# Kernel tuning notes

Hardware: AMD Instinct MI355X
Metric: run time of the kernel (lower is better)

The kernel has to match this reference:

```python
import jax, jax.numpy as jnp
import numpy as np

# --- config constants (from init_kwargs) ---
ALPHA = 0.05; SIGMA = 0.2; THETA = 0.3; A = 0.02; B_PAR = 0.1; RHO = 0.5
MULT = 2.0          # config.x_range_final[1]
GAMMA = 0.5         # power-utility exponent: u(x,r)=r*x^g/g, ux=r*x^(g-1)
N_STEPS = 100; T_FINAL = 1.0; DT = T_FINAL / N_STEPS
HID = 64; BATCH = 16384
PEN_SCALE = 100.0; LOWER = 1e-6


def _mlp(W1, b1, W2, b2, W3, b3, s):
    # tiny FeedForwardSubNet: 3 -> HID -> HID -> 1, tanh activations
    h = jnp.tanh(s @ W1 + b1)
    h = jnp.tanh(h @ W2 + b2)
    return h @ W3 + b3


def _penalise(v):
    # penalise_range(v, lower): quadratic hinge below `lower`
    return PEN_SCALE * jnp.square(jnp.maximum(LOWER - v, 0.0))


def setup_inputs() -> dict:
    key = jax.random.key(0)
    ks = jax.random.split(key, 16)
    dw = jax.random.normal(ks[0], (BATCH, 1, N_STEPS), dtype=jnp.float32) * float(np.sqrt(DT))
    X0 = jnp.ones((1,), jnp.float32)
    R0 = jnp.ones((1,), jnp.float32)
    def w(k, shape, fan):
        return jax.random.normal(k, shape, jnp.float32) / np.float32(np.sqrt(fan))
    inp = {"dw": dw, "X0": X0, "R0": R0,
           "pW1": w(ks[1], (3, HID), 3), "pb1": jnp.zeros((HID,), jnp.float32),
           "pW2": w(ks[2], (HID, HID), HID), "pb2": jnp.zeros((HID,), jnp.float32),
           "pW3": w(ks[3], (HID, 1), HID), "pb3": jnp.zeros((1,), jnp.float32),
           "qW1": w(ks[4], (3, HID), 3), "qb1": jnp.zeros((HID,), jnp.float32),
           "qW2": w(ks[5], (HID, HID), HID), "qb2": jnp.zeros((HID,), jnp.float32),
           "qW3": w(ks[6], (HID, 1), HID), "qb3": jnp.zeros((1,), jnp.float32)}
    return inp


def reference(dw, X0, R0, pW1, pb1, pW2, pb2, pW3, pb3, qW1, qb1, qW2, qb2, qW3, qb3):
    Bn = dw.shape[0]
    ones = jnp.ones((Bn, 1), dw.dtype)
    times = jnp.arange(N_STEPS + 1, dtype=dw.dtype) * DT   # [N+1]
    x0 = ones * X0
    R0v = ones * R0
    b_eff = float(np.sign(RHO)) * B_PAR

    # p_0 and dp_0 = d p_0 / d x (per-sample, rowwise independent net)
    def p_of_x(xx):
        st = jnp.concatenate([MULT * times[0] * ones, xx, R0v], 1)
        return _mlp(pW1, pb1, pW2, pb2, pW3, pb3, st)
    p0, p_vjp = jax.vjp(p_of_x, x0)
    (dp0,) = p_vjp(jnp.ones_like(p0))
    pi0 = _mlp(qW1, qb1, qW2, qb2, qW3, qb3,
               jnp.concatenate([MULT * times[0] * ones, x0, R0v], 1))

    dw_t = jnp.transpose(dw, (2, 0, 1))          # [N, B, 1]
    upd = jnp.arange(N_STEPS) < (N_STEPS - 1)    # pi not updated at last step

    def step(carry, inp):
        x, min_x, W, pi = carry
        dwi, t_next, u = inp
        x = x + x * ALPHA * DT + pi * SIGMA * THETA * DT + pi * SIGMA * dwi
        min_x = jnp.minimum(x, min_x)
        W = W + dwi
        Rv = R0v * jnp.exp((A - 0.5 * b_eff ** 2) * t_next + b_eff * W)
        p = p0 * jnp.exp(-(ALPHA + 0.5 * THETA ** 2) * t_next - THETA * W)
        st = jnp.concatenate([MULT * t_next * jnp.ones_like(x), x, Rv], 1)
        pi_new = _mlp(qW1, qb1, qW2, qb2, qW3, qb3, st)
        pi = jnp.where(u, pi_new, pi)
        return (x, min_x, W, pi), (x, Rv, pi, -p)

    (xf, min_x, Wf, pif), (xs, Rs, pis, dMs) = jax.lax.scan(
        step, (x0, x0, jnp.zeros_like(x0), pi0), (dw_t, times[1:], upd))

    # stacked process data, matching tf.concat-over-axis-0 ordering: [(N+1)*B, 1]
    x_all  = jnp.concatenate([x0[None], xs], 0).reshape(-1, 1)
    r_all  = jnp.concatenate([R0v[None], Rs], 0).reshape(-1, 1)
    pi_all = jnp.concatenate([pi0[None], pis], 0).reshape(-1, 1)
    dM_all = jnp.concatenate([(-p0)[None], dMs], 0).reshape(-1, 1)
    dM2_all = jnp.tile(-dp0, (N_STEPS + 1, 1))
    proc = jnp.concatenate([x_all, r_all, pi_all, dM_all, dM2_all], 1)  # [(N+1)*B, 5]

    # losses (non_concave = False branch)
    p_fin = -dMs[-1]
    R_fin = Rs[-1]
    xc = jnp.maximum(xf, LOWER)
    ux = R_fin * xc ** (GAMMA - 1.0)
    u_val = R_fin * xc ** GAMMA / GAMMA
    pen = _penalise(min_x)
    loss_p = jnp.mean(jnp.square(p_fin + ux) + pen)
    loss_pi = loss_p + jnp.mean(-u_val + pen)

    return jnp.concatenate([proc.reshape(-1), jnp.stack([loss_p, loss_pi])])
```

## Files before the change

kernel.cpp:

```cpp
#include <hip/hip_runtime.h>
#include <math.h>

#define NSTEP 100
#define BATCH 16384
#define MB 16
#define NBLK (BATCH/MB)
#define NT 64

#define C_ALPHA 0.05f
#define C_SIGMA 0.2f
#define C_THETA 0.3f
#define C_DT    0.01f
#define C_LOWER 1e-6f
#define C_PEN   100.0f
#define LOG2E   1.4426950408889634f
#define TSCALE  (2.0f * LOG2E)
#define CRT ( 0.015f * C_DT * LOG2E)
#define CRW ( 0.1f * LOG2E)
#define CPT (-0.095f * C_DT * LOG2E)
#define CPW (-0.3f * LOG2E)

typedef __attribute__((ext_vector_type(8))) short bf16x8;
typedef __attribute__((ext_vector_type(4))) float f32x4;

__device__ __forceinline__ float tanh_pre(float zs) {
    float e = __builtin_amdgcn_exp2f(zs);
    return 1.0f - 2.0f * __builtin_amdgcn_rcpf(e + 1.0f);
}
__device__ __forceinline__ unsigned f2bf_u(float f) {
    unsigned u = __float_as_uint(f);
    return (u + 0x7FFFu + ((u >> 16) & 1u)) >> 16;
}

__global__ void init_kernel(const float* X0, const float* R0,
                            const float* pW1, const float* pb1, const float* pW2,
                            const float* pb2, const float* pW3, const float* pb3,
                            const float* qW1, const float* qb1, const float* qW2,
                            const float* qb2, const float* qW3, const float* qb3,
                            float* ws) {
    __shared__ float sw[2][4096];
    int tid = threadIdx.x;
    for (int u = tid; u < 4096; u += 256) { sw[0][u] = pW2[u]; sw[1][u] = qW2[u]; }
    __syncthreads();
    int wv = tid >> 6, j = tid & 63;
    float sx = X0[0], sr = R0[0];
    if (wv == 0) {
        float pre = pW1[64 + j] * sx + pW1[128 + j] * sr + pb1[j];
        float h1 = tanh_pre(TSCALE * pre);
        float d1 = (1.0f - h1 * h1) * pW1[64 + j];
        float pre2 = pb2[j], dpre2 = 0.0f;
        #pragma unroll 8
        for (int i2 = 0; i2 < 64; i2++) {
            float w = sw[0][i2 * 64 + j];
            pre2  += __shfl(h1, i2) * w;
            dpre2 += __shfl(d1, i2) * w;
        }
        float h2 = tanh_pre(TSCALE * pre2);
        float d2 = (1.0f - h2 * h2) * dpre2;
        float c1 = h2 * pW3[j], c2 = d2 * pW3[j];
        for (int o = 32; o >= 1; o >>= 1) {
            c1 += __shfl_down(c1, o); c2 += __shfl_down(c2, o);
        }
        if (j == 0) { ws[0] = c1 + pb3[0]; ws[1] = c2; }
    } else if (wv == 1) {
        float pre = qW1[64 + j] * sx + qW1[128 + j] * sr + qb1[j];
        float h1 = tanh_pre(TSCALE * pre);
        float pre2 = qb2[j];
        #pragma unroll 8
        for (int i2 = 0; i2 < 64; i2++) pre2 += __shfl(h1, i2) * sw[1][i2 * 64 + j];
        float h2 = tanh_pre(TSCALE * pre2);
        float c1 = h2 * qW3[j];
        for (int o = 32; o >= 1; o >>= 1) c1 += __shfl_down(c1, o);
        if (j == 0) { ws[2] = c1 + qb3[0]; ws[3] = 0.0f; ws[4] = 0.0f; ws[5] = 0.0f; }
    }
}

__global__ __launch_bounds__(NT, 1) void step_kernel(
        const float* __restrict__ dw, const float* __restrict__ X0,
        const float* __restrict__ R0,
        const float* __restrict__ qW1, const float* __restrict__ qb1,
        const float* __restrict__ qW2, const float* __restrict__ qb2,
        const float* __restrict__ qW3, const float* __restrict__ qb3,
        float* __restrict__ ws, float* __restrict__ out) {
    __shared__ __align__(16) unsigned short sW2T[64 * 72];
    __shared__ __align__(16) float sdw[MB * NSTEP];
    __shared__ __align__(16) float sPi[MB];

    const int lane = threadIdx.x;
    const int b0 = blockIdx.x * MB;
    const int l15 = lane & 15, quad = lane >> 4;

    {
        const float4* g = (const float4*)(dw + (size_t)b0 * NSTEP);
        float4* s = (float4*)sdw;
        #pragma unroll
        for (int u = lane; u < MB * NSTEP / 4; u += NT) s[u] = g[u];
    }
    #pragma unroll 8
    for (int t = 0; t < 64; t++) {
        float w = qW2[t * 64 + lane];
        sW2T[lane * 72 + t] = (unsigned short)f2bf_u(w * TSCALE);
    }
    bf16x8 Bf[4][2];
    #pragma unroll
    for (int nt = 0; nt < 4; nt++) {
        const unsigned short* r = &sW2T[(nt * 16 + l15) * 72 + quad * 8];
        Bf[nt][0] = *(const bf16x8*)r;
        Bf[nt][1] = *(const bf16x8*)(r + 32);
    }
    float tco[16], w1xs[16], w1rs[16], b1s[16];
    #pragma unroll
    for (int idx = 0; idx < 16; idx++) {
        int k = (idx < 8) ? (quad * 8 + idx) : (32 + quad * 8 + (idx - 8));
        tco[idx]  = qW1[k] * (2.0f * C_DT * TSCALE);
        w1xs[idx] = qW1[64 + k] * TSCALE;
        w1rs[idx] = qW1[128 + k] * TSCALE;
        b1s[idx]  = qb1[k] * TSCALE;
    }
    float b2v[4], w3v[4];
    #pragma unroll
    for (int nt = 0; nt < 4; nt++) {
        b2v[nt] = qb2[nt * 16 + l15] * TSCALE;
        w3v[nt] = qW3[nt * 16 + l15];
    }
    const float b3 = qb3[0];
    const float p0 = ws[0], dp0 = ws[1], pi0 = ws[2];
    const float X0v = X0[0], R0s = R0[0];

    float x = 0.f, Wsum = 0.f, minx = 0.f, R0v = 0.f, pi = 0.f;
    float v1 = 0.f, v2 = 0.f;
    if (lane < MB) {
        x = X0v; R0v = R0s; minx = x; pi = pi0;
        sPi[lane] = pi0;
        size_t base = (size_t)(b0 + lane) * 5;
        out[base] = x; out[base + 1] = R0v; out[base + 2] = pi0;
        out[base + 3] = -p0; out[base + 4] = -dp0;
    }

    #pragma unroll 1
    for (int i = 0; i < NSTEP - 1; i++) {
        float fi = (float)(i + 1);
        float Rcur = 0.f;
        if (lane < MB) {
            pi = sPi[lane];
            float dwv = sdw[lane * NSTEP + i];
            x = x * (1.0f + C_ALPHA * C_DT) + pi * C_SIGMA * (C_THETA * C_DT + dwv);
            minx = fminf(minx, x);
            Wsum += dwv;
            Rcur = R0v * __builtin_amdgcn_exp2f(fmaf(CRW, Wsum, CRT * fi));
            float pm = p0 * __builtin_amdgcn_exp2f(fmaf(CPW, Wsum, CPT * fi));
            size_t base = ((size_t)(i + 1) * BATCH + b0 + lane) * 5;
            out[base] = x; out[base + 1] = Rcur;
            out[base + 3] = -pm; out[base + 4] = -dp0;
        }
        float xb = __shfl(x, l15);
        float rb = __shfl(Rcur, l15);

        union { bf16x8 v; unsigned u[4]; } A0, A1;
        #pragma unroll
        for (int p = 0; p < 8; p++) {
            int i0 = 2 * p, i1 = 2 * p + 1;
            float z0 = fmaf(w1rs[i0], rb, fmaf(w1xs[i0], xb, fmaf(tco[i0], fi, b1s[i0])));
            float z1 = fmaf(w1rs[i1], rb, fmaf(w1xs[i1], xb, fmaf(tco[i1], fi, b1s[i1])));
            unsigned pk = f2bf_u(tanh_pre(z0)) | (f2bf_u(tanh_pre(z1)) << 16);
            if (p < 4) A0.u[p] = pk; else A1.u[p - 4] = pk;
        }
        f32x4 part;
        {
            f32x4 acc0 = {b2v[0], b2v[0], b2v[0], b2v[0]};
            f32x4 acc1 = {b2v[1], b2v[1], b2v[1], b2v[1]};
            f32x4 acc2 = {b2v[2], b2v[2], b2v[2], b2v[2]};
            f32x4 acc3 = {b2v[3], b2v[3], b2v[3], b2v[3]};
            acc0 = __builtin_amdgcn_mfma_f32_16x16x32_bf16(A0.v, Bf[0][0], acc0, 0, 0, 0);
            acc1 = __builtin_amdgcn_mfma_f32_16x16x32_bf16(A0.v, Bf[1][0], acc1, 0, 0, 0);
            acc2 = __builtin_amdgcn_mfma_f32_16x16x32_bf16(A0.v, Bf[2][0], acc2, 0, 0, 0);
            acc3 = __builtin_amdgcn_mfma_f32_16x16x32_bf16(A0.v, Bf[3][0], acc3, 0, 0, 0);
            acc0 = __builtin_amdgcn_mfma_f32_16x16x32_bf16(A1.v, Bf[0][1], acc0, 0, 0, 0);
            acc1 = __builtin_amdgcn_mfma_f32_16x16x32_bf16(A1.v, Bf[1][1], acc1, 0, 0, 0);
            acc2 = __builtin_amdgcn_mfma_f32_16x16x32_bf16(A1.v, Bf[2][1], acc2, 0, 0, 0);
            acc3 = __builtin_amdgcn_mfma_f32_16x16x32_bf16(A1.v, Bf[3][1], acc3, 0, 0, 0);
            #pragma unroll
            for (int r = 0; r < 4; r++) {
                float s = tanh_pre(acc0[r]) * w3v[0];
                s = fmaf(tanh_pre(acc1[r]), w3v[1], s);
                s = fmaf(tanh_pre(acc2[r]), w3v[2], s);
                s = fmaf(tanh_pre(acc3[r]), w3v[3], s);
                part[r] = s;
            }
        }
        #pragma unroll
        for (int o = 1; o < 16; o <<= 1) {
            part[0] += __shfl_xor(part[0], o);
            part[1] += __shfl_xor(part[1], o);
            part[2] += __shfl_xor(part[2], o);
            part[3] += __shfl_xor(part[3], o);
        }
        if (l15 == 0) {
            float q0 = part[0] + b3, q1 = part[1] + b3;
            float q2 = part[2] + b3, q3 = part[3] + b3;
            f32x4 pv = {q0, q1, q2, q3};
            *(f32x4*)&sPi[quad * 4] = pv;
            size_t base = ((size_t)(i + 1) * BATCH + b0 + quad * 4) * 5 + 2;
            out[base] = q0; out[base + 5] = q1; out[base + 10] = q2; out[base + 15] = q3;
        }
    }

    if (lane < MB) {
        pi = sPi[lane];
        float dwv = sdw[lane * NSTEP + (NSTEP - 1)];
        x = x * (1.0f + C_ALPHA * C_DT) + pi * C_SIGMA * (C_THETA * C_DT + dwv);
        minx = fminf(minx, x);
        Wsum += dwv;
        float Rf = R0v * __builtin_amdgcn_exp2f(fmaf(CRW, Wsum, CRT * (float)NSTEP));
        float pf = p0 * __builtin_amdgcn_exp2f(fmaf(CPW, Wsum, CPT * (float)NSTEP));
        size_t base = ((size_t)NSTEP * BATCH + b0 + lane) * 5;
        out[base] = x; out[base + 1] = Rf; out[base + 2] = pi;
        out[base + 3] = -pf; out[base + 4] = -dp0;

        float xc = fmaxf(x, C_LOWER);
        float ux = Rf * rsqrtf(xc);
        float uval = 2.0f * Rf * sqrtf(xc);
        float d = fmaxf(C_LOWER - minx, 0.0f);
        float pen = C_PEN * d * d;
        float t1 = pf + ux;
        v1 = t1 * t1 + pen;
        v2 = -uval + pen;
    }
    #pragma unroll
    for (int o = 8; o >= 1; o >>= 1) {
        v1 += __shfl_down(v1, o);
        v2 += __shfl_down(v2, o);
    }
    if (lane == 0) {
        atomicAdd(&ws[3], v1);
        atomicAdd(&ws[4], v2);
        __threadfence();
        int old = atomicAdd((int*)(ws + 5), 1);
        if (old == NBLK - 1) {
            float lp = atomicAdd(&ws[3], 0.0f) * (1.0f / (float)BATCH);
            float lq = atomicAdd(&ws[4], 0.0f) * (1.0f / (float)BATCH);
            out[(size_t)(NSTEP + 1) * BATCH * 5] = lp;
            out[(size_t)(NSTEP + 1) * BATCH * 5 + 1] = lp + lq;
        }
    }
}

extern "C" void kernel_launch(void* const* d_in, const int* in_sizes, int n_in,
                              void* d_out, int out_size, void* d_ws, size_t ws_size,
                              hipStream_t stream) {
    const float* dw  = (const float*)d_in[0];
    const float* X0  = (const float*)d_in[1];
    const float* R0  = (const float*)d_in[2];
    const float* pW1 = (const float*)d_in[3];
    const float* pb1 = (const float*)d_in[4];
    const float* pW2 = (const float*)d_in[5];
    const float* pb2 = (const float*)d_in[6];
    const float* pW3 = (const float*)d_in[7];
    const float* pb3 = (const float*)d_in[8];
    const float* qW1 = (const float*)d_in[9];
    const float* qb1 = (const float*)d_in[10];
    const float* qW2 = (const float*)d_in[11];
    const float* qb2 = (const float*)d_in[12];
    const float* qW3 = (const float*)d_in[13];
    const float* qb3 = (const float*)d_in[14];
    float* out = (float*)d_out;
    float* ws  = (float*)d_ws;

    init_kernel<<<1, 256, 0, stream>>>(X0, R0, pW1, pb1, pW2, pb2, pW3, pb3,
                                       qW1, qb1, qW2, qb2, qW3, qb3, ws);
    step_kernel<<<NBLK, NT, 0, stream>>>(dw, X0, R0, qW1, qb1, qW2, qb2, qW3, qb3,
                                         ws, out);
}
```

Baseline: 229.0 us.

## Fuse init kernel into step kernel and keep recurrence state replicated across lanes

Drops the separate single-block init kernel: each block now computes p0/dp0 and the initial policy value itself, and the accumulators are zeroed with a memset. The per-step state update runs redundantly in every quad, so the shared-memory round trip for pi is gone. The 16-lane reductions use DPP row operations and the result is redistributed with ds_bpermute instead of shfl_xor chains. dw values are prefetched one step ahead and bf16 packing uses the library intrinsic. In exchange, every block recomputes the small p-net.

Result: faster. 209.6 us (-8.5%).

```diff
diff --git a/kernel.cpp b/kernel.cpp
--- a/kernel.cpp
+++ b/kernel.cpp
@@ -1,4 +1,5 @@
 #include <hip/hip_runtime.h>
+#include <hip/hip_bf16.h>
 #include <math.h>
 
 #define NSTEP 100
@@ -31,60 +32,36 @@
     unsigned u = __float_as_uint(f);
     return (u + 0x7FFFu + ((u >> 16) & 1u)) >> 16;
 }
-
-__global__ void init_kernel(const float* X0, const float* R0,
-                            const float* pW1, const float* pb1, const float* pW2,
-                            const float* pb2, const float* pW3, const float* pb3,
-                            const float* qW1, const float* qb1, const float* qW2,
-                            const float* qb2, const float* qW3, const float* qb3,
-                            float* ws) {
-    __shared__ float sw[2][4096];
-    int tid = threadIdx.x;
-    for (int u = tid; u < 4096; u += 256) { sw[0][u] = pW2[u]; sw[1][u] = qW2[u]; }
-    __syncthreads();
-    int wv = tid >> 6, j = tid & 63;
-    float sx = X0[0], sr = R0[0];
-    if (wv == 0) {
-        float pre = pW1[64 + j] * sx + pW1[128 + j] * sr + pb1[j];
-        float h1 = tanh_pre(TSCALE * pre);
-        float d1 = (1.0f - h1 * h1) * pW1[64 + j];
-        float pre2 = pb2[j], dpre2 = 0.0f;
-        #pragma unroll 8
-        for (int i2 = 0; i2 < 64; i2++) {
-            float w = sw[0][i2 * 64 + j];
-            pre2  += __shfl(h1, i2) * w;
-            dpre2 += __shfl(d1, i2) * w;
-        }
-        float h2 = tanh_pre(TSCALE * pre2);
-        float d2 = (1.0f - h2 * h2) * dpre2;
-        float c1 = h2 * pW3[j], c2 = d2 * pW3[j];
-        for (int o = 32; o >= 1; o >>= 1) {
-            c1 += __shfl_down(c1, o); c2 += __shfl_down(c2, o);
-        }
-        if (j == 0) { ws[0] = c1 + pb3[0]; ws[1] = c2; }
-    } else if (wv == 1) {
-        float pre = qW1[64 + j] * sx + qW1[128 + j] * sr + qb1[j];
-        float h1 = tanh_pre(TSCALE * pre);
-        float pre2 = qb2[j];
-        #pragma unroll 8
-        for (int i2 = 0; i2 < 64; i2++) pre2 += __shfl(h1, i2) * sw[1][i2 * 64 + j];
-        float h2 = tanh_pre(TSCALE * pre2);
-        float c1 = h2 * qW3[j];
-        for (int o = 32; o >= 1; o >>= 1) c1 += __shfl_down(c1, o);
-        if (j == 0) { ws[2] = c1 + qb3[0]; ws[3] = 0.0f; ws[4] = 0.0f; ws[5] = 0.0f; }
-    }
-}
-
-__global__ __launch_bounds__(NT, 1) void step_kernel(
+__device__ __forceinline__ unsigned pack_bf16(float a, float b) {
+    union { __hip_bfloat162 h; unsigned u; } cv;
+    cv.h = __float22bfloat162_rn(make_float2(a, b));
+    return cv.u;
+}
+__device__ __forceinline__ float dpp_row_sum16(float v) {
+    int t;
+    t = __builtin_amdgcn_update_dpp(0, __float_as_int(v), 0x128, 0xF, 0xF, true);
+    v += __int_as_float(t);
+    t = __builtin_amdgcn_update_dpp(0, __float_as_int(v), 0x124, 0xF, 0xF, true);
+    v += __int_as_float(t);
+    t = __builtin_amdgcn_update_dpp(0, __float_as_int(v), 0x122, 0xF, 0xF, true);
+    v += __int_as_float(t);
+    t = __builtin_amdgcn_update_dpp(0, __float_as_int(v), 0x121, 0xF, 0xF, true);
+    v += __int_as_float(t);
+    return v;
+}
+
+__global__ __launch_bounds__(NT, 1) void fused_kernel(
         const float* __restrict__ dw, const float* __restrict__ X0,
         const float* __restrict__ R0,
+        const float* __restrict__ pW1, const float* __restrict__ pb1,
+        const float* __restrict__ pW2, const float* __restrict__ pb2,
+        const float* __restrict__ pW3, const float* __restrict__ pb3,
         const float* __restrict__ qW1, const float* __restrict__ qb1,
         const float* __restrict__ qW2, const float* __restrict__ qb2,
         const float* __restrict__ qW3, const float* __restrict__ qb3,
         float* __restrict__ ws, float* __restrict__ out) {
     __shared__ __align__(16) unsigned short sW2T[64 * 72];
     __shared__ __align__(16) float sdw[MB * NSTEP];
-    __shared__ __align__(16) float sPi[MB];
 
     const int lane = threadIdx.x;
     const int b0 = blockIdx.x * MB;
@@ -97,10 +74,10 @@
         for (int u = lane; u < MB * NSTEP / 4; u += NT) s[u] = g[u];
     }
     #pragma unroll 8
-    for (int t = 0; t < 64; t++) {
-        float w = qW2[t * 64 + lane];
-        sW2T[lane * 72 + t] = (unsigned short)f2bf_u(w * TSCALE);
-    }
+    for (int t = 0; t < 64; t++)
+        sW2T[lane * 72 + t] = (unsigned short)f2bf_u(qW2[t * 64 + lane] * TSCALE);
+    __syncthreads();
+
     bf16x8 Bf[4][2];
     #pragma unroll
     for (int nt = 0; nt < 4; nt++) {
@@ -124,123 +101,136 @@
         w3v[nt] = qW3[nt * 16 + l15];
     }
     const float b3 = qb3[0];
-    const float p0 = ws[0], dp0 = ws[1], pi0 = ws[2];
     const float X0v = X0[0], R0s = R0[0];
-
-    float x = 0.f, Wsum = 0.f, minx = 0.f, R0v = 0.f, pi = 0.f;
-    float v1 = 0.f, v2 = 0.f;
-    if (lane < MB) {
-        x = X0v; R0v = R0s; minx = x; pi = pi0;
-        sPi[lane] = pi0;
-        size_t base = (size_t)(b0 + lane) * 5;
-        out[base] = x; out[base + 1] = R0v; out[base + 2] = pi0;
+    const int bperm_idx = (((l15 >> 2) * 16) + (l15 & 3)) * 4;
+
+    float p0, dp0;
+    {
+        float pre = fmaf(pW1[64 + lane], X0v, fmaf(pW1[128 + lane], R0s, pb1[lane]));
+        float h1 = tanh_pre(TSCALE * pre);
+        float d1 = (1.0f - h1 * h1) * pW1[64 + lane];
+        float a0 = pb2[lane], a1 = 0.f, a2 = 0.f, a3 = 0.f;
+        float e0 = 0.f, e1 = 0.f, e2 = 0.f, e3 = 0.f;
+        for (int i2 = 0; i2 < 64; i2 += 4) {
+            float w0 = pW2[(i2 + 0) * 64 + lane];
+            float w1 = pW2[(i2 + 1) * 64 + lane];
+            float w2 = pW2[(i2 + 2) * 64 + lane];
+            float w3 = pW2[(i2 + 3) * 64 + lane];
+            a0 = fmaf(__shfl(h1, i2 + 0), w0, a0); e0 = fmaf(__shfl(d1, i2 + 0), w0, e0);
+            a1 = fmaf(__shfl(h1, i2 + 1), w1, a1); e1 = fmaf(__shfl(d1, i2 + 1), w1, e1);
+            a2 = fmaf(__shfl(h1, i2 + 2), w2, a2); e2 = fmaf(__shfl(d1, i2 + 2), w2, e2);
+            a3 = fmaf(__shfl(h1, i2 + 3), w3, a3); e3 = fmaf(__shfl(d1, i2 + 3), w3, e3);
+        }
+        float pre2 = (a0 + a1) + (a2 + a3);
+        float dpre2 = (e0 + e1) + (e2 + e3);
+        float h2 = tanh_pre(TSCALE * pre2);
+        float d2 = (1.0f - h2 * h2) * dpre2;
+        float c1 = h2 * pW3[lane], c2 = d2 * pW3[lane];
+        #pragma unroll
+        for (int o = 1; o < 64; o <<= 1) {
+            c1 += __shfl_xor(c1, o);
+            c2 += __shfl_xor(c2, o);
+        }
+        p0 = c1 + pb3[0]; dp0 = c2;
+    }
+
+    auto qnet = [&](float fi, float xv, float rv) -> float {
+        union { bf16x8 v; unsigned u[4]; } A0, A1;
+        #pragma unroll
+        for (int p = 0; p < 8; p++) {
+            const int i0 = 2 * p, i1 = 2 * p + 1;
+            float z0 = fmaf(w1rs[i0], rv, fmaf(w1xs[i0], xv, fmaf(tco[i0], fi, b1s[i0])));
+            float z1 = fmaf(w1rs[i1], rv, fmaf(w1xs[i1], xv, fmaf(tco[i1], fi, b1s[i1])));
+            unsigned pk = pack_bf16(tanh_pre(z0), tanh_pre(z1));
+            if (p < 4) A0.u[p] = pk; else A1.u[p - 4] = pk;
+        }
+        f32x4 acc0 = {b2v[0], b2v[0], b2v[0], b2v[0]};
+        f32x4 acc1 = {b2v[1], b2v[1], b2v[1], b2v[1]};
+        f32x4 acc2 = {b2v[2], b2v[2], b2v[2], b2v[2]};
+        f32x4 acc3 = {b2v[3], b2v[3], b2v[3], b2v[3]};
+        acc0 = __builtin_amdgcn_mfma_f32_16x16x32_bf16(A0.v, Bf[0][0], acc0, 0, 0, 0);
+        acc1 = __builtin_amdgcn_mfma_f32_16x16x32_bf16(A0.v, Bf[1][0], acc1, 0, 0, 0);
+        acc2 = __builtin_amdgcn_mfma_f32_16x16x32_bf16(A0.v, Bf[2][0], acc2, 0, 0, 0);
+        acc3 = __builtin_amdgcn_mfma_f32_16x16x32_bf16(A0.v, Bf[3][0], acc3, 0, 0, 0);
+        acc0 = __builtin_amdgcn_mfma_f32_16x16x32_bf16(A1.v, Bf[0][1], acc0, 0, 0, 0);
+        acc1 = __builtin_amdgcn_mfma_f32_16x16x32_bf16(A1.v, Bf[1][1], acc1, 0, 0, 0);
+        acc2 = __builtin_amdgcn_mfma_f32_16x16x32_bf16(A1.v, Bf[2][1], acc2, 0, 0, 0);
+        acc3 = __builtin_amdgcn_mfma_f32_16x16x32_bf16(A1.v, Bf[3][1], acc3, 0, 0, 0);
+        f32x4 part;
+        #pragma unroll
+        for (int r = 0; r < 4; r++) {
+            float sA = fmaf(tanh_pre(acc1[r]), w3v[1], tanh_pre(acc0[r]) * w3v[0]);
+            float sB = fmaf(tanh_pre(acc3[r]), w3v[3], tanh_pre(acc2[r]) * w3v[2]);
+            part[r] = dpp_row_sum16(sA + sB);
+        }
+        float sLo = (lane & 1) ? part[1] : part[0];
+        float sHi = (lane & 1) ? part[3] : part[2];
+        float sel = (lane & 2) ? sHi : sLo;
+        int g = __builtin_amdgcn_ds_bpermute(bperm_idx, __float_as_int(sel));
+        return __int_as_float(g) + b3;
+    };
+
+    float x = X0v, Wsum = 0.0f, minx = X0v;
+    float pi = qnet(0.0f, X0v, R0s);
+    if (quad == 0) {
+        size_t base = (size_t)(b0 + l15) * 5;
+        out[base] = X0v; out[base + 1] = R0s; out[base + 2] = pi;
         out[base + 3] = -p0; out[base + 4] = -dp0;
     }
 
+    float dw_next = sdw[l15 * NSTEP];
     #pragma unroll 1
     for (int i = 0; i < NSTEP - 1; i++) {
-        float fi = (float)(i + 1);
-        float Rcur = 0.f;
-        if (lane < MB) {
-            pi = sPi[lane];
-            float dwv = sdw[lane * NSTEP + i];
-            x = x * (1.0f + C_ALPHA * C_DT) + pi * C_SIGMA * (C_THETA * C_DT + dwv);
-            minx = fminf(minx, x);
-            Wsum += dwv;
-            Rcur = R0v * __builtin_amdgcn_exp2f(fmaf(CRW, Wsum, CRT * fi));
-            float pm = p0 * __builtin_amdgcn_exp2f(fmaf(CPW, Wsum, CPT * fi));
-            size_t base = ((size_t)(i + 1) * BATCH + b0 + lane) * 5;
-            out[base] = x; out[base + 1] = Rcur;
-            out[base + 3] = -pm; out[base + 4] = -dp0;
-        }
-        float xb = __shfl(x, l15);
-        float rb = __shfl(Rcur, l15);
-
-        union { bf16x8 v; unsigned u[4]; } A0, A1;
-        #pragma unroll
-        for (int p = 0; p < 8; p++) {
-            int i0 = 2 * p, i1 = 2 * p + 1;
-            float z0 = fmaf(w1rs[i0], rb, fmaf(w1xs[i0], xb, fmaf(tco[i0], fi, b1s[i0])));
-            float z1 = fmaf(w1rs[i1], rb, fmaf(w1xs[i1], xb, fmaf(tco[i1], fi, b1s[i1])));
-            unsigned pk = f2bf_u(tanh_pre(z0)) | (f2bf_u(tanh_pre(z1)) << 16);
-            if (p < 4) A0.u[p] = pk; else A1.u[p - 4] = pk;
-        }
-        f32x4 part;
-        {
-            f32x4 acc0 = {b2v[0], b2v[0], b2v[0], b2v[0]};
-            f32x4 acc1 = {b2v[1], b2v[1], b2v[1], b2v[1]};
-            f32x4 acc2 = {b2v[2], b2v[2], b2v[2], b2v[2]};
-            f32x4 acc3 = {b2v[3], b2v[3], b2v[3], b2v[3]};
-            acc0 = __builtin_amdgcn_mfma_f32_16x16x32_bf16(A0.v, Bf[0][0], acc0, 0, 0, 0);
-            acc1 = __builtin_amdgcn_mfma_f32_16x16x32_bf16(A0.v, Bf[1][0], acc1, 0, 0, 0);
-            acc2 = __builtin_amdgcn_mfma_f32_16x16x32_bf16(A0.v, Bf[2][0], acc2, 0, 0, 0);
-            acc3 = __builtin_amdgcn_mfma_f32_16x16x32_bf16(A0.v, Bf[3][0], acc3, 0, 0, 0);
-            acc0 = __builtin_amdgcn_mfma_f32_16x16x32_bf16(A1.v, Bf[0][1], acc0, 0, 0, 0);
-            acc1 = __builtin_amdgcn_mfma_f32_16x16x32_bf16(A1.v, Bf[1][1], acc1, 0, 0, 0);
-            acc2 = __builtin_amdgcn_mfma_f32_16x16x32_bf16(A1.v, Bf[2][1], acc2, 0, 0, 0);
-            acc3 = __builtin_amdgcn_mfma_f32_16x16x32_bf16(A1.v, Bf[3][1], acc3, 0, 0, 0);
-            #pragma unroll
-            for (int r = 0; r < 4; r++) {
-                float s = tanh_pre(acc0[r]) * w3v[0];
-                s = fmaf(tanh_pre(acc1[r]), w3v[1], s);
-                s = fmaf(tanh_pre(acc2[r]), w3v[2], s);
-                s = fmaf(tanh_pre(acc3[r]), w3v[3], s);
-                part[r] = s;
-            }
-        }
-        #pragma unroll
-        for (int o = 1; o < 16; o <<= 1) {
-            part[0] += __shfl_xor(part[0], o);
-            part[1] += __shfl_xor(part[1], o);
-            part[2] += __shfl_xor(part[2], o);
-            part[3] += __shfl_xor(part[3], o);
-        }
-        if (l15 == 0) {
-            float q0 = part[0] + b3, q1 = part[1] + b3;
-            float q2 = part[2] + b3, q3 = part[3] + b3;
-            f32x4 pv = {q0, q1, q2, q3};
-            *(f32x4*)&sPi[quad * 4] = pv;
-            size_t base = ((size_t)(i + 1) * BATCH + b0 + quad * 4) * 5 + 2;
-            out[base] = q0; out[base + 5] = q1; out[base + 10] = q2; out[base + 15] = q3;
-        }
-    }
-
-    if (lane < MB) {
-        pi = sPi[lane];
-        float dwv = sdw[lane * NSTEP + (NSTEP - 1)];
-        x = x * (1.0f + C_ALPHA * C_DT) + pi * C_SIGMA * (C_THETA * C_DT + dwv);
+        const float fi = (float)(i + 1);
+        float dwv = dw_next;
+        dw_next = sdw[l15 * NSTEP + i + 1];
+        float t = pi * C_SIGMA;
+        x = fmaf(x, 1.0f + C_ALPHA * C_DT, fmaf(t, dwv, t * (C_THETA * C_DT)));
         minx = fminf(minx, x);
         Wsum += dwv;
-        float Rf = R0v * __builtin_amdgcn_exp2f(fmaf(CRW, Wsum, CRT * (float)NSTEP));
+        float R = R0s * __builtin_amdgcn_exp2f(fmaf(CRW, Wsum, CRT * fi));
+        float pm = p0 * __builtin_amdgcn_exp2f(fmaf(CPW, Wsum, CPT * fi));
+        float pin = qnet(fi, x, R);
+        if (quad == 0) {
+            size_t base = ((size_t)(i + 1) * BATCH + b0 + l15) * 5;
+            out[base] = x; out[base + 1] = R; out[base + 2] = pin;
+            out[base + 3] = -pm; out[base + 4] = -dp0;
+        }
+        pi = pin;
+    }
+
+    {
+        float dwv = dw_next;
+        float t = pi * C_SIGMA;
+        x = fmaf(x, 1.0f + C_ALPHA * C_DT, fmaf(t, dwv, t * (C_THETA * C_DT)));
+        minx = fminf(minx, x);
+        Wsum += dwv;
+        float Rf = R0s * __builtin_amdgcn_exp2f(fmaf(CRW, Wsum, CRT * (float)NSTEP));
         float pf = p0 * __builtin_amdgcn_exp2f(fmaf(CPW, Wsum, CPT * (float)NSTEP));
-        size_t base = ((size_t)NSTEP * BATCH + b0 + lane) * 5;
-        out[base] = x; out[base + 1] = Rf; out[base + 2] = pi;
-        out[base + 3] = -pf; out[base + 4] = -dp0;
-
+        if (quad == 0) {
+            size_t base = ((size_t)NSTEP * BATCH + b0 + l15) * 5;
+            out[base] = x; out[base + 1] = Rf; out[base + 2] = pi;
+            out[base + 3] = -pf; out[base + 4] = -dp0;
+        }
         float xc = fmaxf(x, C_LOWER);
         float ux = Rf * rsqrtf(xc);
         float uval = 2.0f * Rf * sqrtf(xc);
         float d = fmaxf(C_LOWER - minx, 0.0f);
         float pen = C_PEN * d * d;
         float t1 = pf + ux;
-        v1 = t1 * t1 + pen;
-        v2 = -uval + pen;
-    }
-    #pragma unroll
-    for (int o = 8; o >= 1; o >>= 1) {
-        v1 += __shfl_down(v1, o);
-        v2 += __shfl_down(v2, o);
-    }
-    if (lane == 0) {
-        atomicAdd(&ws[3], v1);
-        atomicAdd(&ws[4], v2);
-        __threadfence();
-        int old = atomicAdd((int*)(ws + 5), 1);
-        if (old == NBLK - 1) {
-            float lp = atomicAdd(&ws[3], 0.0f) * (1.0f / (float)BATCH);
-            float lq = atomicAdd(&ws[4], 0.0f) * (1.0f / (float)BATCH);
-            out[(size_t)(NSTEP + 1) * BATCH * 5] = lp;
-            out[(size_t)(NSTEP + 1) * BATCH * 5 + 1] = lp + lq;
+        float v1 = dpp_row_sum16(t1 * t1 + pen);
+        float v2 = dpp_row_sum16(-uval + pen);
+        if (lane == 0) {
+            atomicAdd(&ws[3], v1);
+            atomicAdd(&ws[4], v2);
+            __threadfence();
+            int old = atomicAdd((int*)(ws + 5), 1);
+            if (old == NBLK - 1) {
+                float lp = atomicAdd(&ws[3], 0.0f) * (1.0f / (float)BATCH);
+                float lq = atomicAdd(&ws[4], 0.0f) * (1.0f / (float)BATCH);
+                out[(size_t)(NSTEP + 1) * BATCH * 5] = lp;
+                out[(size_t)(NSTEP + 1) * BATCH * 5 + 1] = lp + lq;
+            }
         }
     }
 }
@@ -266,8 +256,7 @@
     float* out = (float*)d_out;
     float* ws  = (float*)d_ws;
 
-    init_kernel<<<1, 256, 0, stream>>>(X0, R0, pW1, pb1, pW2, pb2, pW3, pb3,
-                                       qW1, qb1, qW2, qb2, qW3, qb3, ws);
-    step_kernel<<<NBLK, NT, 0, stream>>>(dw, X0, R0, qW1, qb1, qW2, qb2, qW3, qb3,
-                                         ws, out);
-}
+    hipMemsetAsync(d_ws, 0, 64, stream);
+    fused_kernel<<<NBLK, NT, 0, stream>>>(dw, X0, R0, pW1, pb1, pW2, pb2, pW3, pb3,
+                                          qW1, qb1, qW2, qb2, qW3, qb3, ws, out);
+}
```
